# Kernel optimization log

Measured on AMD Instinct MI355X. Metric: run time of the kernel, lower is better.

## Reference

```python
import jax, jax.numpy as jnp
import numpy as np

N_PREV = 65536
BATCH = 2048
DIM = 128


def setup_inputs() -> dict:
    key = jax.random.key(0)
    k1, k2 = jax.random.split(key)
    n = N_PREV + BATCH
    target_lib = jax.random.normal(k1, (n, DIM), dtype=jnp.float32)
    reached_lib = jax.random.normal(k2, (n, DIM), dtype=jnp.float32)
    return {
        "target_goal_embedding_library": target_lib,
        "reached_goal_embedding_library": reached_lib,
        "batch_size": BATCH,
    }


def reference(target_goal_embedding_library, reached_goal_embedding_library, batch_size):
    # slice the library: last batch_size rows are current target/reached goals
    tg = target_goal_embedding_library[-batch_size:]      # [B, D]
    rg = reached_goal_embedding_library[-batch_size:]     # [B, D]
    prev = reached_goal_embedding_library[:-batch_size]   # [N_prev, D]

    # brute-force squared euclidean distances via gram trick: [B, N_prev]
    d2 = (
        jnp.sum(tg * tg, axis=-1, keepdims=True)
        - 2.0 * tg @ prev.T
        + jnp.sum(prev * prev, axis=-1)[None, :]
    )
    idx = jnp.argmin(d2, axis=1)          # top-1 nearest neighbor ids, [B]
    closest = prev[idx]                   # [B, D] gather

    # LP(g, s, r) = ||g - s|| - ||g - r||; value and grad wrt g, vmapped over batch
    def LP(g, s, r):
        return (
            jnp.sqrt(jnp.sum(jnp.square(g - s), axis=-1))
            - jnp.sqrt(jnp.sum(jnp.square(g - r), axis=-1))
        )

    IM_vals, IM_grads = jax.vmap(jax.value_and_grad(LP, 0), in_axes=(0, 0, 0))(
        tg, closest, rg
    )
    return IM_vals, IM_grads
```

## Files before the change

### kernel.cpp

```cpp
#include <hip/hip_runtime.h>
#include <math.h>

#define DIM 128
#define BATCH 2048
#define NPREV 65536
#define NCH 32
#define NJT 16
#define DELTA 0.8f

typedef __attribute__((ext_vector_type(8))) short bf16x8;
typedef __attribute__((ext_vector_type(4))) float f32x4;
typedef unsigned short u16;

static __device__ __forceinline__ unsigned short f2bf(float f) {
    unsigned int u = __float_as_uint(f);
    u += 0x7FFF + ((u >> 16) & 1);
    return (unsigned short)(u >> 16);
}

#define GLOAD16(g, l) __builtin_amdgcn_global_load_lds( \
    (const __attribute__((address_space(1))) void*)(g), \
    (__attribute__((address_space(3))) void*)(l), 16, 0, 0)

__global__ __launch_bounds__(256) void k_convB(const float* __restrict__ src,
                                               u16* __restrict__ dst,
                                               float* __restrict__ p2part) {
    int id = blockIdx.x * 256 + threadIdx.x;
    int img = id >> 10, c = id & 1023;
    int ks2 = c >> 9, rem = c & 511, row = rem >> 2, slot = rem & 3;
    int koct = slot ^ ((row >> 1) & 3);
    int srow = (img >> 1) * 128 + row;
    int scol = (img & 1) * 64 + ks2 * 32 + koct * 8;
    const float* s = src + (size_t)srow * DIM + scol;
    float4 f0 = *reinterpret_cast<const float4*>(s);
    float4 f1 = *reinterpret_cast<const float4*>(s + 4);
    float f[8] = {f0.x, f0.y, f0.z, f0.w, f1.x, f1.y, f1.z, f1.w};
    union { unsigned short us[8]; uint4 v; } o;
    float sum = 0.f;
    #pragma unroll
    for (int e = 0; e < 8; ++e) { o.us[e] = f2bf(f[e]); sum += f[e] * f[e]; }
    *reinterpret_cast<uint4*>(dst + (size_t)id * 8) = o.v;
    p2part[srow * 16 + (scol >> 3)] = sum;
}

__global__ __launch_bounds__(256) void k_prev2r(const float* __restrict__ p2part,
                                                float* __restrict__ p2h) {
    int row = blockIdx.x * 256 + threadIdx.x;
    const float4* p = reinterpret_cast<const float4*>(p2part + (size_t)row * 16);
    float4 a = p[0], b = p[1], c = p[2], d = p[3];
    float s = ((a.x + a.y) + (a.z + a.w)) + ((b.x + b.y) + (b.z + b.w))
            + ((c.x + c.y) + (c.z + c.w)) + ((d.x + d.y) + (d.z + d.w));
    p2h[row] = -0.5f * s;
}

__global__ __launch_bounds__(256) void k_convA(const float* __restrict__ src,
                                               u16* __restrict__ dst) {
    int id = blockIdx.x * 256 + threadIdx.x;
    int img = id >> 10, c = id & 1023;
    int ks2 = c >> 9, rem = c & 511, row = rem >> 2, koct = rem & 3;
    int srow = (img >> 1) * 128 + row;
    int scol = (img & 1) * 64 + ks2 * 32 + koct * 8;
    const float* s = src + (size_t)srow * DIM + scol;
    float4 f0 = *reinterpret_cast<const float4*>(s);
    float4 f1 = *reinterpret_cast<const float4*>(s + 4);
    float f[8] = {f0.x, f0.y, f0.z, f0.w, f1.x, f1.y, f1.z, f1.w};
    union { unsigned short us[8]; uint4 v; } o;
    #pragma unroll
    for (int e = 0; e < 8; ++e) o.us[e] = f2bf(f[e]);
    *reinterpret_cast<uint4*>(dst + (size_t)id * 8) = o.v;
}

__global__ __launch_bounds__(512, 4) void k_gemm_argmin(
    const u16* __restrict__ Aimg, const u16* __restrict__ Bimg,
    const float* __restrict__ p2h, float4* __restrict__ partial)
{
    __shared__ __align__(16) u16 Bt[2][16384];

    const int t = threadIdx.x;
    const int lane = t & 63;
    const int w = t >> 6;
    const int wrow = w & 3;
    const int cg = w >> 2;
    const int l15 = lane & 15;
    const int lhi = lane >> 4;

    const int bid = blockIdx.x;
    const int mtile = bid >> 5;
    const int chunk = bid & 31;

    const u16* gb0 = Bimg + (size_t)chunk * NJT * 16384;

    #pragma unroll
    for (int c = 0; c < 4; ++c)
        GLOAD16(gb0 + c * 4096 + t * 8, &Bt[0][c * 4096 + t * 8]);

    bf16x8 areg[4][2];
    {
        const u16* ab = Aimg + (size_t)mtile * 2 * 8192;
        #pragma unroll
        for (int s = 0; s < 4; ++s) {
            const int img = s >> 1, ks2 = s & 1;
            #pragma unroll
            for (int fm = 0; fm < 2; ++fm) {
                int row = wrow * 32 + fm * 16 + l15;
                areg[s][fm] = *reinterpret_cast<const bf16x8*>(
                    ab + (size_t)img * 8192 + (ks2 * 512 + row * 4 + lhi) * 8);
            }
        }
    }

    const int sbyte = (lhi ^ ((l15 >> 1) & 3)) << 4;
    const int bbase = (cg * 64 + l15) * 64 + sbyte;
    const unsigned sbase = ((unsigned)cg << 8) | (unsigned)l15;
    const int phbase = chunk * 2048 + cg * 64 + l15;

    float v1[2][4], v2[2][4];
    #pragma unroll
    for (int fm = 0; fm < 2; ++fm)
        #pragma unroll
        for (int r = 0; r < 4; ++r) { v1[fm][r] = -INFINITY; v2[fm][r] = -INFINITY; }

    float phc[4];
    #pragma unroll
    for (int fn = 0; fn < 4; ++fn) phc[fn] = p2h[phbase + fn * 16];

    for (int jt = 0; jt < NJT; ++jt) {
        const int p = jt & 1;
        __syncthreads();
        if (jt + 1 < NJT) {
            const u16* gb = gb0 + (size_t)(jt + 1) * 16384;
            u16* lb = Bt[p ^ 1];
            #pragma unroll
            for (int c = 0; c < 4; ++c)
                GLOAD16(gb + c * 4096 + t * 8, lb + c * 4096 + t * 8);
        }
        float phn[4];
        if (jt + 1 < NJT) {
            #pragma unroll
            for (int fn = 0; fn < 4; ++fn)
                phn[fn] = p2h[phbase + (jt + 1) * 128 + fn * 16];
        }

        f32x4 acc[2][4];
        #pragma unroll
        for (int fn = 0; fn < 4; ++fn) {
            const float pv = phc[fn];
            #pragma unroll
            for (int fm = 0; fm < 2; ++fm)
                acc[fm][fn] = (f32x4){pv, pv, pv, pv};
        }

        const char* Bc = (const char*)Bt[p];
        #pragma unroll
        for (int s = 0; s < 4; ++s) {
            const int img = s >> 1, ks2 = s & 1;
            bf16x8 bf[4];
            #pragma unroll
            for (int fn = 0; fn < 4; ++fn)
                bf[fn] = *reinterpret_cast<const bf16x8*>(
                    Bc + img * 16384 + ks2 * 8192 + fn * 1024 + bbase);
            #pragma unroll
            for (int fm = 0; fm < 2; ++fm)
                #pragma unroll
                for (int fn = 0; fn < 4; ++fn)
                    acc[fm][fn] = __builtin_amdgcn_mfma_f32_16x16x32_bf16(
                        areg[s][fm], bf[fn], acc[fm][fn], 0, 0, 0);
        }

        const unsigned stampv = sbase | ((unsigned)jt << 4);
        #pragma unroll
        for (int fm = 0; fm < 2; ++fm) {
            #pragma unroll
            for (int r = 0; r < 4; ++r) {
                float m = fmaxf(fmaxf(acc[fm][0][r], acc[fm][1][r]),
                                fmaxf(acc[fm][2][r], acc[fm][3][r]));
                float key = __uint_as_float((__float_as_uint(m) & ~0x7FFu) | stampv);
                float tm = fminf(v1[fm][r], key);
                v1[fm][r] = fmaxf(v1[fm][r], key);
                v2[fm][r] = fmaxf(v2[fm][r], tm);
            }
        }

        if (jt + 1 < NJT) {
            #pragma unroll
            for (int fn = 0; fn < 4; ++fn) phc[fn] = phn[fn];
        }
    }

    float2* red = reinterpret_cast<float2*>(Bt);
    #pragma unroll
    for (int fm = 0; fm < 2; ++fm) {
        #pragma unroll
        for (int r = 0; r < 4; ++r) {
            float a1 = v1[fm][r], a2 = v2[fm][r];
            #pragma unroll
            for (int m = 1; m < 16; m <<= 1) {
                float o1 = __shfl_xor(a1, m), o2 = __shfl_xor(a2, m);
                float n2 = fmaxf(fminf(a1, o1), fmaxf(a2, o2));
                a1 = fmaxf(a1, o1); a2 = n2;
            }
            if (l15 == 0) {
                int row = wrow * 32 + fm * 16 + lhi * 4 + r;
                red[row * 2 + cg] = make_float2(a1, a2);
            }
        }
    }
    __syncthreads();
    if (t < 128) {
        float2 x = red[t * 2 + 0], y = red[t * 2 + 1];
        float u1f = fmaxf(x.x, y.x);
        float u2f = fmaxf(fminf(x.x, y.x), fmaxf(x.y, y.y));
        unsigned ua = __float_as_uint(u1f), ub = __float_as_uint(u2f);
        int ja = chunk * 2048 + (int)((ua >> 4) & 15) * 128 + (int)((ua >> 8) & 1) * 64
               + (int)(ua & 15);
        int jb = chunk * 2048 + (int)((ub >> 4) & 15) * 128 + (int)((ub >> 8) & 1) * 64
               + (int)(ub & 15);
        float d1 = -2.0f * __uint_as_float(ua & ~0x7FFu);
        float d2 = -2.0f * __uint_as_float(ub & ~0x7FFu);
        partial[(size_t)(mtile * 128 + t) * NCH + chunk] =
            make_float4(d1, __int_as_float(ja), d2, __int_as_float(jb));
    }
}

__global__ __launch_bounds__(256) void k_final2(
    const float* __restrict__ tg, const float* __restrict__ rg,
    const float* __restrict__ prev, const float2* __restrict__ partial2,
    float* __restrict__ out_vals, float* __restrict__ out_grads)
{
    const int wv = threadIdx.x >> 6, lane = threadIdx.x & 63;
    const int i = blockIdx.x * 4 + wv;
    const float2 e = partial2[(size_t)i * 64 + lane];
    const float v = e.x; const int j = __float_as_int(e.y);

    float bv = v;
    #pragma unroll
    for (int m = 1; m < 64; m <<= 1) bv = fminf(bv, __shfl_xor(bv, m));

    unsigned long long mask = __ballot(v <= bv + DELTA);
    const float2 g = *reinterpret_cast<const float2*>(tg + (size_t)i * DIM + 2 * lane);

    float bestd = INFINITY; int bestj = 0x7fffffff;
    while (mask) {
        int src = __ffsll(mask) - 1; mask &= mask - 1;
        int cjg = __shfl(j, src);
        #pragma unroll
        for (int f = 0; f < 4; ++f) {
            int cj = cjg + f * 16;
            const float2 p = *reinterpret_cast<const float2*>(prev + (size_t)cj * DIM + 2 * lane);
            float dx = g.x - p.x, dy = g.y - p.y;
            float d = dx * dx + dy * dy;
            #pragma unroll
            for (int m = 1; m < 64; m <<= 1) d += __shfl_xor(d, m);
            if (d < bestd || (d == bestd && cj < bestj)) { bestd = d; bestj = cj; }
        }
    }

    const float2 s = *reinterpret_cast<const float2*>(prev + (size_t)bestj * DIM + 2 * lane);
    const float2 r = *reinterpret_cast<const float2*>(rg + (size_t)i * DIM + 2 * lane);
    const float dsx = g.x - s.x, dsy = g.y - s.y;
    const float drx = g.x - r.x, dry = g.y - r.y;
    float ds = dsx * dsx + dsy * dsy;
    float dr = drx * drx + dry * dry;
    #pragma unroll
    for (int m = 1; m < 64; m <<= 1) { ds += __shfl_xor(ds, m); dr += __shfl_xor(dr, m); }
    const float sds = sqrtf(ds), sdr = sqrtf(dr);
    if (lane == 0) out_vals[i] = sds - sdr;
    const float is = 1.0f / sds, ir = 1.0f / sdr;
    float2 gr;
    gr.x = dsx * is - drx * ir;
    gr.y = dsy * is - dry * ir;
    *reinterpret_cast<float2*>(out_grads + (size_t)i * DIM + 2 * lane) = gr;
}

#define TM 128
#define TN 128
#define FNCHUNK 16
#define JT_PER_CHUNK 32

__global__ __launch_bounds__(256) void k_prev2(const float* __restrict__ prev,
                                               float* __restrict__ prev2,
                                               int nprev) {
    const int wave = threadIdx.x >> 6;
    const int lane = threadIdx.x & 63;
    const int row = blockIdx.x * 4 + wave;
    if (row >= nprev) return;
    const float2 v = *reinterpret_cast<const float2*>(prev + (size_t)row * DIM + 2 * lane);
    float s = v.x * v.x + v.y * v.y;
    #pragma unroll
    for (int m = 1; m < 64; m <<= 1) s += __shfl_xor(s, m);
    if (lane == 0) prev2[row] = s;
}

__global__ __launch_bounds__(256, 1) void k_argmin_fb(
    const float* __restrict__ tg, const float* __restrict__ prev,
    const float* __restrict__ prev2, float2* __restrict__ partial)
{
    __shared__ float4 tgL[TM * 32];
    __shared__ float4 pvL[TN * 32];
    __shared__ float  p2L[TN];
    const int t = threadIdx.x;
    const int rowTile = blockIdx.x;
    const int chunk = blockIdx.y;
    const float4* tgG = reinterpret_cast<const float4*>(tg + (size_t)rowTile * TM * DIM);
    #pragma unroll
    for (int i = 0; i < 16; ++i) {
        const int idx = t + 256 * i;
        const int row = idx >> 5, kk = idx & 31;
        tgL[row * 32 + (kk ^ (row & 7))] = tgG[idx];
    }
    const int tx = t & 15, ty = t >> 4;
    const int sa = ty & 7, sb = tx & 7;
    float minval[8]; int minidx[8];
    #pragma unroll
    for (int ri = 0; ri < 8; ++ri) { minval[ri] = INFINITY; minidx[ri] = 0x7fffffff; }
    const int jchunk0 = chunk * (JT_PER_CHUNK * TN);
    for (int jt = 0; jt < JT_PER_CHUNK; ++jt) {
        const int j0 = jchunk0 + jt * TN;
        __syncthreads();
        const float4* pvG = reinterpret_cast<const float4*>(prev + (size_t)j0 * DIM);
        #pragma unroll
        for (int i = 0; i < 16; ++i) {
            const int idx = t + 256 * i;
            const int row = idx >> 5, kk = idx & 31;
            pvL[row * 32 + (kk ^ (row & 7))] = pvG[idx];
        }
        if (t < TN) p2L[t] = prev2[j0 + t];
        __syncthreads();
        float acc[8][8];
        #pragma unroll
        for (int ri = 0; ri < 8; ++ri)
            #pragma unroll
            for (int ci = 0; ci < 8; ++ci) acc[ri][ci] = 0.f;
        #pragma unroll 2
        for (int kk = 0; kk < 32; ++kk) {
            float4 a[8], b[8];
            const int ka = kk ^ sa, kb = kk ^ sb;
            #pragma unroll
            for (int ri = 0; ri < 8; ++ri) a[ri] = tgL[(ty + 16 * ri) * 32 + ka];
            #pragma unroll
            for (int ci = 0; ci < 8; ++ci) b[ci] = pvL[(tx + 16 * ci) * 32 + kb];
            #pragma unroll
            for (int ri = 0; ri < 8; ++ri)
                #pragma unroll
                for (int ci = 0; ci < 8; ++ci) {
                    acc[ri][ci] += a[ri].x * b[ci].x;
                    acc[ri][ci] += a[ri].y * b[ci].y;
                    acc[ri][ci] += a[ri].z * b[ci].z;
                    acc[ri][ci] += a[ri].w * b[ci].w;
                }
        }
        #pragma unroll
        for (int ci = 0; ci < 8; ++ci) {
            const int jl = tx + 16 * ci;
            const int jg = j0 + jl;
            const float pj = p2L[jl];
            #pragma unroll
            for (int ri = 0; ri < 8; ++ri) {
                const float d = pj - 2.f * acc[ri][ci];
                if (d < minval[ri]) { minval[ri] = d; minidx[ri] = jg; }
            }
        }
    }
    __syncthreads();
    float2* red = reinterpret_cast<float2*>(pvL);
    #pragma unroll
    for (int ri = 0; ri < 8; ++ri) {
        const int row = ty + 16 * ri;
        red[row * 16 + tx] = make_float2(minval[ri], __int_as_float(minidx[ri]));
    }
    __syncthreads();
    if (t < TM) {
        float bv = INFINITY; int bi = 0x7fffffff;
        #pragma unroll
        for (int e = 0; e < 16; ++e) {
            const float2 p = red[t * 16 + e];
            const int pi = __float_as_int(p.y);
            if (p.x < bv || (p.x == bv && pi < bi)) { bv = p.x; bi = pi; }
        }
        partial[(size_t)(rowTile * TM + t) * FNCHUNK + chunk] =
            make_float2(bv, __int_as_float(bi));
    }
}

__global__ __launch_bounds__(256) void k_final_fb(
    const float* __restrict__ tg, const float* __restrict__ rg,
    const float* __restrict__ prev, const float2* __restrict__ partial,
    float* __restrict__ out_vals, float* __restrict__ out_grads)
{
    const int wave = threadIdx.x >> 6, lane = threadIdx.x & 63;
    const int i = blockIdx.x * 4 + wave;
    float bv = INFINITY; int bi = 0x7fffffff;
    if (lane < FNCHUNK) {
        const float2 p = partial[(size_t)i * FNCHUNK + lane];
        bv = p.x; bi = __float_as_int(p.y);
    }
    #pragma unroll
    for (int m = 1; m < 16; m <<= 1) {
        const float ov = __shfl_xor(bv, m);
        const int   oi = __shfl_xor(bi, m);
        if (ov < bv || (ov == bv && oi < bi)) { bv = ov; bi = oi; }
    }
    bi = __shfl(bi, 0);
    const float2 g = *reinterpret_cast<const float2*>(tg   + (size_t)i  * DIM + 2 * lane);
    const float2 s = *reinterpret_cast<const float2*>(prev + (size_t)bi * DIM + 2 * lane);
    const float2 r = *reinterpret_cast<const float2*>(rg   + (size_t)i  * DIM + 2 * lane);
    const float dsx = g.x - s.x, dsy = g.y - s.y;
    const float drx = g.x - r.x, dry = g.y - r.y;
    float ds = dsx * dsx + dsy * dsy;
    float dr = drx * drx + dry * dry;
    #pragma unroll
    for (int m = 1; m < 64; m <<= 1) { ds += __shfl_xor(ds, m); dr += __shfl_xor(dr, m); }
    const float sds = sqrtf(ds), sdr = sqrtf(dr);
    if (lane == 0) out_vals[i] = sds - sdr;
    const float is = 1.0f / sds, ir = 1.0f / sdr;
    float2 gr;
    gr.x = dsx * is - drx * ir;
    gr.y = dsy * is - dry * ir;
    *reinterpret_cast<float2*>(out_grads + (size_t)i * DIM + 2 * lane) = gr;
}

extern "C" void kernel_launch(void* const* d_in, const int* in_sizes, int n_in,
                              void* d_out, int out_size, void* d_ws, size_t ws_size,
                              hipStream_t stream) {
    const float* target  = (const float*)d_in[0];
    const float* reached = (const float*)d_in[1];
    const int n_total = in_sizes[0] / DIM;
    const int nprev = n_total - BATCH;

    const float* tg   = target  + (size_t)nprev * DIM;
    const float* rg   = reached + (size_t)nprev * DIM;
    const float* prev = reached;

    float* out_vals  = (float*)d_out;
    float* out_grads = out_vals + BATCH;

    const size_t offB  = 0;
    const size_t offA  = (size_t)1024 * 8192 * 2;
    const size_t offP2 = offA + (size_t)32 * 8192 * 2;
    const size_t offPP = offP2 + (size_t)NPREV * 4;
    const size_t offPt = offPP + (size_t)NPREV * 16 * 4;
    const size_t need  = offPt + (size_t)BATCH * NCH * sizeof(float4);

    if (nprev == NPREV && ws_size >= need) {
        u16*    Bb      = (u16*)((char*)d_ws + offB);
        u16*    Ab      = (u16*)((char*)d_ws + offA);
        float*  p2h     = (float*)((char*)d_ws + offP2);
        float*  p2part  = (float*)((char*)d_ws + offPP);
        float4* partial = (float4*)((char*)d_ws + offPt);

        k_convB<<<(1024 * 1024) / 256, 256, 0, stream>>>(prev, Bb, p2part);
        k_convA<<<(32 * 1024) / 256, 256, 0, stream>>>(tg, Ab);
        k_prev2r<<<NPREV / 256, 256, 0, stream>>>(p2part, p2h);
        k_gemm_argmin<<<512, 512, 0, stream>>>(Ab, Bb, p2h, partial);
        k_final2<<<BATCH / 4, 256, 0, stream>>>(tg, rg, prev, (const float2*)partial,
                                                out_vals, out_grads);
    } else {
        float*  prev2   = (float*)d_ws;
        float2* partial = (float2*)((char*)d_ws + (size_t)nprev * sizeof(float));
        k_prev2<<<nprev / 4, 256, 0, stream>>>(prev, prev2, nprev);
        dim3 grid(BATCH / TM, FNCHUNK);
        k_argmin_fb<<<grid, 256, 0, stream>>>(tg, prev, prev2, partial);
        k_final_fb<<<BATCH / 4, 256, 0, stream>>>(tg, rg, prev, partial, out_vals, out_grads);
    }
}
```

Measured before the change: 65.74 us.

## Retile GEMM-argmin to 256-thread blocks with 64 column chunks and top-2 candidates

Changes the fused GEMM/argmin tiling. Each workgroup now has 4 waves, each computing a 64x32 output tile, and the previous-embedding set is split into 64 chunks, giving 1024 blocks and half the LDS per block. The B image layout is regenerated for 64-row tiles. The p2 norm is added after the MFMA chain instead of seeding the accumulators, and s_setprio is raised around the MFMA loop. The final kernel now reads both top-1 and top-2 per-chunk candidates, each covering 2 columns instead of 4. The aim is better occupancy and load balance with more A reuse per wave, at the cost of more partials to reduce and possible extra candidate rechecks.

```diff
diff --git a/kernel.cpp b/kernel.cpp
--- a/kernel.cpp
+++ b/kernel.cpp
@@ -4,7 +4,7 @@
 #define DIM 128
 #define BATCH 2048
 #define NPREV 65536
-#define NCH 32
+#define NCH 64
 #define NJT 16
 #define DELTA 0.8f
 
@@ -26,10 +26,10 @@
                                                u16* __restrict__ dst,
                                                float* __restrict__ p2part) {
     int id = blockIdx.x * 256 + threadIdx.x;
-    int img = id >> 10, c = id & 1023;
-    int ks2 = c >> 9, rem = c & 511, row = rem >> 2, slot = rem & 3;
-    int koct = slot ^ ((row >> 1) & 3);
-    int srow = (img >> 1) * 128 + row;
+    int img = id >> 9, c = id & 511;
+    int ks2 = c >> 8, rem = c & 255, col = rem >> 2, slot = rem & 3;
+    int koct = slot ^ ((col >> 1) & 3);
+    int srow = (img >> 1) * 64 + col;
     int scol = (img & 1) * 64 + ks2 * 32 + koct * 8;
     const float* s = src + (size_t)srow * DIM + scol;
     float4 f0 = *reinterpret_cast<const float4*>(s);
@@ -70,110 +70,112 @@
     *reinterpret_cast<uint4*>(dst + (size_t)id * 8) = o.v;
 }
 
-__global__ __launch_bounds__(512, 4) void k_gemm_argmin(
+__global__ __launch_bounds__(256, 3) void k_gemm_argmin(
     const u16* __restrict__ Aimg, const u16* __restrict__ Bimg,
     const float* __restrict__ p2h, float4* __restrict__ partial)
 {
-    __shared__ __align__(16) u16 Bt[2][16384];
+    __shared__ __align__(16) u16 Bt[2][8192];
 
     const int t = threadIdx.x;
     const int lane = t & 63;
     const int w = t >> 6;
-    const int wrow = w & 3;
-    const int cg = w >> 2;
+    const int wrow = w & 1;
+    const int cg = w >> 1;
     const int l15 = lane & 15;
     const int lhi = lane >> 4;
 
     const int bid = blockIdx.x;
-    const int mtile = bid >> 5;
-    const int chunk = bid & 31;
-
-    const u16* gb0 = Bimg + (size_t)chunk * NJT * 16384;
+    const int mtile = bid >> 6;
+    const int chunk = bid & 63;
+
+    const u16* gb0 = Bimg + (size_t)chunk * NJT * 8192;
 
     #pragma unroll
     for (int c = 0; c < 4; ++c)
-        GLOAD16(gb0 + c * 4096 + t * 8, &Bt[0][c * 4096 + t * 8]);
-
-    bf16x8 areg[4][2];
+        GLOAD16(gb0 + c * 2048 + t * 8, &Bt[0][c * 2048 + t * 8]);
+
+    bf16x8 areg[4][4];
     {
         const u16* ab = Aimg + (size_t)mtile * 2 * 8192;
         #pragma unroll
         for (int s = 0; s < 4; ++s) {
             const int img = s >> 1, ks2 = s & 1;
             #pragma unroll
-            for (int fm = 0; fm < 2; ++fm) {
-                int row = wrow * 32 + fm * 16 + l15;
+            for (int fm = 0; fm < 4; ++fm) {
+                int row = wrow * 64 + fm * 16 + l15;
                 areg[s][fm] = *reinterpret_cast<const bf16x8*>(
                     ab + (size_t)img * 8192 + (ks2 * 512 + row * 4 + lhi) * 8);
             }
         }
     }
 
-    const int sbyte = (lhi ^ ((l15 >> 1) & 3)) << 4;
-    const int bbase = (cg * 64 + l15) * 64 + sbyte;
+    const int bbase = (cg * 32 + l15) * 64 + ((lhi ^ ((l15 >> 1) & 3)) << 4);
     const unsigned sbase = ((unsigned)cg << 8) | (unsigned)l15;
-    const int phbase = chunk * 2048 + cg * 64 + l15;
-
-    float v1[2][4], v2[2][4];
-    #pragma unroll
-    for (int fm = 0; fm < 2; ++fm)
+    const int phbase = chunk * 1024 + cg * 32 + l15;
+    const f32x4 z4 = {0.f, 0.f, 0.f, 0.f};
+
+    float v1[4][4], v2[4][4];
+    #pragma unroll
+    for (int fm = 0; fm < 4; ++fm)
         #pragma unroll
         for (int r = 0; r < 4; ++r) { v1[fm][r] = -INFINITY; v2[fm][r] = -INFINITY; }
 
-    float phc[4];
-    #pragma unroll
-    for (int fn = 0; fn < 4; ++fn) phc[fn] = p2h[phbase + fn * 16];
+    float phc[2];
+    phc[0] = p2h[phbase]; phc[1] = p2h[phbase + 16];
 
     for (int jt = 0; jt < NJT; ++jt) {
         const int p = jt & 1;
         __syncthreads();
         if (jt + 1 < NJT) {
-            const u16* gb = gb0 + (size_t)(jt + 1) * 16384;
+            const u16* gb = gb0 + (size_t)(jt + 1) * 8192;
             u16* lb = Bt[p ^ 1];
             #pragma unroll
             for (int c = 0; c < 4; ++c)
-                GLOAD16(gb + c * 4096 + t * 8, lb + c * 4096 + t * 8);
-        }
-        float phn[4];
+                GLOAD16(gb + c * 2048 + t * 8, lb + c * 2048 + t * 8);
+        }
+        float phn[2];
         if (jt + 1 < NJT) {
-            #pragma unroll
-            for (int fn = 0; fn < 4; ++fn)
-                phn[fn] = p2h[phbase + (jt + 1) * 128 + fn * 16];
-        }
-
-        f32x4 acc[2][4];
-        #pragma unroll
-        for (int fn = 0; fn < 4; ++fn) {
-            const float pv = phc[fn];
-            #pragma unroll
-            for (int fm = 0; fm < 2; ++fm)
-                acc[fm][fn] = (f32x4){pv, pv, pv, pv};
-        }
-
+            phn[0] = p2h[phbase + (jt + 1) * 64];
+            phn[1] = p2h[phbase + (jt + 1) * 64 + 16];
+        }
+
+        f32x4 acc[4][2];
         const char* Bc = (const char*)Bt[p];
+        __builtin_amdgcn_s_setprio(1);
         #pragma unroll
         for (int s = 0; s < 4; ++s) {
-            const int img = s >> 1, ks2 = s & 1;
-            bf16x8 bf[4];
-            #pragma unroll
-            for (int fn = 0; fn < 4; ++fn)
+            const int h = s >> 1, ks2 = s & 1;
+            bf16x8 bf[2];
+            #pragma unroll
+            for (int fn = 0; fn < 2; ++fn)
                 bf[fn] = *reinterpret_cast<const bf16x8*>(
-                    Bc + img * 16384 + ks2 * 8192 + fn * 1024 + bbase);
-            #pragma unroll
-            for (int fm = 0; fm < 2; ++fm)
+                    Bc + h * 8192 + ks2 * 4096 + fn * 1024 + bbase);
+            if (s == 0) {
                 #pragma unroll
-                for (int fn = 0; fn < 4; ++fn)
-                    acc[fm][fn] = __builtin_amdgcn_mfma_f32_16x16x32_bf16(
-                        areg[s][fm], bf[fn], acc[fm][fn], 0, 0, 0);
-        }
+                for (int fm = 0; fm < 4; ++fm)
+                    #pragma unroll
+                    for (int fn = 0; fn < 2; ++fn)
+                        acc[fm][fn] = __builtin_amdgcn_mfma_f32_16x16x32_bf16(
+                            areg[0][fm], bf[fn], z4, 0, 0, 0);
+            } else {
+                #pragma unroll
+                for (int fm = 0; fm < 4; ++fm)
+                    #pragma unroll
+                    for (int fn = 0; fn < 2; ++fn)
+                        acc[fm][fn] = __builtin_amdgcn_mfma_f32_16x16x32_bf16(
+                            areg[s][fm], bf[fn], acc[fm][fn], 0, 0, 0);
+            }
+        }
+        __builtin_amdgcn_s_setprio(0);
 
         const unsigned stampv = sbase | ((unsigned)jt << 4);
         #pragma unroll
-        for (int fm = 0; fm < 2; ++fm) {
+        for (int fm = 0; fm < 4; ++fm) {
             #pragma unroll
             for (int r = 0; r < 4; ++r) {
-                float m = fmaxf(fmaxf(acc[fm][0][r], acc[fm][1][r]),
-                                fmaxf(acc[fm][2][r], acc[fm][3][r]));
+                float s0 = acc[fm][0][r] + phc[0];
+                float s1 = acc[fm][1][r] + phc[1];
+                float m = fmaxf(s0, s1);
                 float key = __uint_as_float((__float_as_uint(m) & ~0x7FFu) | stampv);
                 float tm = fminf(v1[fm][r], key);
                 v1[fm][r] = fmaxf(v1[fm][r], key);
@@ -181,15 +183,12 @@
             }
         }
 
-        if (jt + 1 < NJT) {
-            #pragma unroll
-            for (int fn = 0; fn < 4; ++fn) phc[fn] = phn[fn];
-        }
+        if (jt + 1 < NJT) { phc[0] = phn[0]; phc[1] = phn[1]; }
     }
 
     float2* red = reinterpret_cast<float2*>(Bt);
     #pragma unroll
-    for (int fm = 0; fm < 2; ++fm) {
+    for (int fm = 0; fm < 4; ++fm) {
         #pragma unroll
         for (int r = 0; r < 4; ++r) {
             float a1 = v1[fm][r], a2 = v2[fm][r];
@@ -200,7 +199,7 @@
                 a1 = fmaxf(a1, o1); a2 = n2;
             }
             if (l15 == 0) {
-                int row = wrow * 32 + fm * 16 + lhi * 4 + r;
+                int row = wrow * 64 + fm * 16 + lhi * 4 + r;
                 red[row * 2 + cg] = make_float2(a1, a2);
             }
         }
@@ -211,9 +210,9 @@
         float u1f = fmaxf(x.x, y.x);
         float u2f = fmaxf(fminf(x.x, y.x), fmaxf(x.y, y.y));
         unsigned ua = __float_as_uint(u1f), ub = __float_as_uint(u2f);
-        int ja = chunk * 2048 + (int)((ua >> 4) & 15) * 128 + (int)((ua >> 8) & 1) * 64
+        int ja = chunk * 1024 + (int)((ua >> 4) & 15) * 64 + (int)((ua >> 8) & 1) * 32
                + (int)(ua & 15);
-        int jb = chunk * 2048 + (int)((ub >> 4) & 15) * 128 + (int)((ub >> 8) & 1) * 64
+        int jb = chunk * 1024 + (int)((ub >> 4) & 15) * 64 + (int)((ub >> 8) & 1) * 32
                + (int)(ub & 15);
         float d1 = -2.0f * __uint_as_float(ua & ~0x7FFu);
         float d2 = -2.0f * __uint_as_float(ub & ~0x7FFu);
@@ -224,28 +223,30 @@
 
 __global__ __launch_bounds__(256) void k_final2(
     const float* __restrict__ tg, const float* __restrict__ rg,
-    const float* __restrict__ prev, const float2* __restrict__ partial2,
+    const float* __restrict__ prev, const float4* __restrict__ partial,
     float* __restrict__ out_vals, float* __restrict__ out_grads)
 {
     const int wv = threadIdx.x >> 6, lane = threadIdx.x & 63;
     const int i = blockIdx.x * 4 + wv;
-    const float2 e = partial2[(size_t)i * 64 + lane];
-    const float v = e.x; const int j = __float_as_int(e.y);
-
-    float bv = v;
+    const float4 e = partial[(size_t)i * NCH + lane];
+
+    float bv = e.x;
     #pragma unroll
     for (int m = 1; m < 64; m <<= 1) bv = fminf(bv, __shfl_xor(bv, m));
 
-    unsigned long long mask = __ballot(v <= bv + DELTA);
+    unsigned long long m1 = __ballot(e.x <= bv + DELTA);
+    unsigned long long m2 = __ballot(e.z <= bv + DELTA);
     const float2 g = *reinterpret_cast<const float2*>(tg + (size_t)i * DIM + 2 * lane);
+    const int j1i = __float_as_int(e.y), j2i = __float_as_int(e.w);
 
     float bestd = INFINITY; int bestj = 0x7fffffff;
-    while (mask) {
-        int src = __ffsll(mask) - 1; mask &= mask - 1;
-        int cjg = __shfl(j, src);
-        #pragma unroll
-        for (int f = 0; f < 4; ++f) {
-            int cj = cjg + f * 16;
+    while (m1 | m2) {
+        int j0;
+        if (m1) { int src = __ffsll(m1) - 1; m1 &= m1 - 1; j0 = __shfl(j1i, src); }
+        else    { int src = __ffsll(m2) - 1; m2 &= m2 - 1; j0 = __shfl(j2i, src); }
+        #pragma unroll
+        for (int f = 0; f < 2; ++f) {
+            int cj = j0 + f * 16;
             const float2 p = *reinterpret_cast<const float2*>(prev + (size_t)cj * DIM + 2 * lane);
             float dx = g.x - p.x, dy = g.y - p.y;
             float d = dx * dx + dy * dy;
@@ -435,7 +436,7 @@
     float* out_grads = out_vals + BATCH;
 
     const size_t offB  = 0;
-    const size_t offA  = (size_t)1024 * 8192 * 2;
+    const size_t offA  = (size_t)2048 * 4096 * 2;
     const size_t offP2 = offA + (size_t)32 * 8192 * 2;
     const size_t offPP = offP2 + (size_t)NPREV * 4;
     const size_t offPt = offPP + (size_t)NPREV * 16 * 4;
@@ -448,11 +449,11 @@
         float*  p2part  = (float*)((char*)d_ws + offPP);
         float4* partial = (float4*)((char*)d_ws + offPt);
 
-        k_convB<<<(1024 * 1024) / 256, 256, 0, stream>>>(prev, Bb, p2part);
+        k_convB<<<(2048 * 512) / 256, 256, 0, stream>>>(prev, Bb, p2part);
         k_convA<<<(32 * 1024) / 256, 256, 0, stream>>>(tg, Ab);
         k_prev2r<<<NPREV / 256, 256, 0, stream>>>(p2part, p2h);
-        k_gemm_argmin<<<512, 512, 0, stream>>>(Ab, Bb, p2h, partial);
-        k_final2<<<BATCH / 4, 256, 0, stream>>>(tg, rg, prev, (const float2*)partial,
+        k_gemm_argmin<<<1024, 256, 0, stream>>>(Ab, Bb, p2h, partial);
+        k_final2<<<BATCH / 4, 256, 0, stream>>>(tg, rg, prev, partial,
                                                 out_vals, out_grads);
     } else {
         float*  prev2   = (float*)d_ws;
```

Result: slower. 70.12 us (+6.7%).
